# Kernel optimization log

Measured on AMD Instinct MI355X. Metric: run time of the kernel, lower is better.

Reference implementation:

```python
import jax, jax.numpy as jnp
import numpy as np

B, S, EMB, H = 2, 2048, 1024, 16
D = EMB // H  # per-head dim = 64
SCALE = 1.0 / np.sqrt(D).astype(np.float32)


def setup_inputs() -> dict:
    key = jax.random.key(0)
    ks = jax.random.split(key, 11)
    lim = 1.0 / np.sqrt(EMB).astype(np.float32)  # torch Linear default init range
    def lin(kw, kb):
        W = jax.random.uniform(kw, (EMB, EMB), jnp.float32, -lim, lim)
        b = jax.random.uniform(kb, (EMB,), jnp.float32, -lim, lim)
        return W, b
    Wq, bq = lin(ks[0], ks[1])
    Wk, bk = lin(ks[2], ks[3])
    Wv, bv = lin(ks[4], ks[5])
    Wo, bo = lin(ks[6], ks[7])
    xq = jax.random.normal(ks[8], (B, S, EMB), jnp.float32)
    xk = jax.random.normal(ks[9], (B, S, EMB), jnp.float32)
    xv = jax.random.normal(ks[10], (B, S, EMB), jnp.float32)
    mask = jnp.tril(jnp.ones((S, S), dtype=jnp.int32))  # causal mask; 0 -> blocked
    return {"xq": xq, "xk": xk, "xv": xv, "mask": mask,
            "Wq": Wq, "bq": bq, "Wk": Wk, "bk": bk,
            "Wv": Wv, "bv": bv, "Wo": Wo, "bo": bo}


def reference(xq, xk, xv, mask, Wq, bq, Wk, bk, Wv, bv, Wo, bo):
    # Projections (torch Linear: x @ W.T + b), then split heads: [B,S,E] -> [B,H,S,D]
    def split_heads(x):
        return x.reshape(B, S, H, D).transpose(0, 2, 1, 3)
    Q = split_heads(xq @ Wq.T + bq)
    K = split_heads(xk @ Wk.T + bk)
    V = split_heads(xv @ Wv.T + bv)
    scores = jnp.einsum("bhqd,bhkd->bhqk", Q, K) * SCALE  # [B,H,S,S]
    scores = jnp.where(mask[None, None, :, :] == 0, jnp.float32(-1e9), scores)
    attn = jax.nn.softmax(scores, axis=-1)  # softmax over key axis (dim=2 per-head in torch)
    res = jnp.einsum("bhqk,bhkd->bhqd", attn, V)
    res = res.transpose(0, 2, 1, 3).reshape(B, S, EMB)  # merge heads back (same slicing layout)
    return res @ Wo.T + bo
```

## Files before the change

### kernel.cpp

```cpp
#include <hip/hip_runtime.h>
#include <hip/hip_bf16.h>

#define BB   2
#define SS   2048
#define EMBD 1024
#define NH   16
#define HD   64
#define QSCALE 0.18033688011112042f
#define NEG_BIG (-1e30f)

typedef __bf16 bf16;
typedef float  floatx4 __attribute__((ext_vector_type(4)));
typedef __bf16 bf16x4  __attribute__((ext_vector_type(4)));
typedef __bf16 bf16x8  __attribute__((ext_vector_type(8)));

typedef const __attribute__((address_space(1))) void* gas_ptr;
typedef __attribute__((address_space(3))) void*       las_ptr;

__device__ __forceinline__ void gl_lds16(const void* g, void* l) {
    __builtin_amdgcn_global_load_lds((gas_ptr)g, (las_ptr)l, 16, 0, 0);
}

__device__ __forceinline__ bf16x8 cvt8(const float* p) {
    bf16x8 o;
#pragma unroll
    for (int j = 0; j < 8; j++) o[j] = (bf16)p[j];
    return o;
}

__global__ __launch_bounds__(256) void cvt_all(
    const float* __restrict__ xq, const float* __restrict__ xk,
    const float* __restrict__ xv, const float* __restrict__ Wq,
    const float* __restrict__ Wk, const float* __restrict__ Wv,
    const float* __restrict__ Wo, bf16* __restrict__ xqo,
    bf16* __restrict__ xko, bf16* __restrict__ xvo, bf16* __restrict__ Wqo,
    bf16* __restrict__ Wko, bf16* __restrict__ Wvo, bf16* __restrict__ Woo) {
    const int y = blockIdx.y;
    const float* src;
    bf16* dst;
    size_t n;
    const size_t NX = (size_t)BB * SS * EMBD;
    const size_t NW = (size_t)EMBD * EMBD;
    switch (y) {
        case 0: src = xq; dst = xqo; n = NX; break;
        case 1: src = xk; dst = xko; n = NX; break;
        case 2: src = xv; dst = xvo; n = NX; break;
        case 3: src = Wq; dst = Wqo; n = NW; break;
        case 4: src = Wk; dst = Wko; n = NW; break;
        case 5: src = Wv; dst = Wvo; n = NW; break;
        default: src = Wo; dst = Woo; n = NW; break;
    }
    const size_t stride = (size_t)gridDim.x * blockDim.x * 4;
    for (size_t i = ((size_t)blockIdx.x * blockDim.x + threadIdx.x) * 4;
         i < n; i += stride) {
        floatx4 v = *(const floatx4*)(src + i);
        bf16x4 o = {(bf16)v[0], (bf16)v[1], (bf16)v[2], (bf16)v[3]};
        *(bf16x4*)(dst + i) = o;
    }
}

extern __shared__ __align__(16) char smem[];

template <int MODE, int FM>
__device__ __forceinline__ void gemm_body(const bf16* __restrict__ A,
                                          const bf16* __restrict__ W,
                                          const float* __restrict__ bias,
                                          void* __restrict__ Ov,
                                          int mBase, int nBase, float oscale) {
    constexpr int BM = 32 * FM;
    constexpr int ABYTES = BM * 64 * 2;
    bf16* As = (bf16*)smem;
    bf16* Bs = (bf16*)(smem + ABYTES);

    const int t = threadIdx.x;
    const int l = t & 63, w = t >> 6;
    const int lm = l & 15, lq = l >> 4;
    const int K = 1024;
    const int wm = (w >> 1) * (16 * FM), wn = (w & 1) * 64;

    const floatx4 zero = {0.f, 0.f, 0.f, 0.f};
    floatx4 acc[FM][4];
#pragma unroll
    for (int i = 0; i < FM; i++)
#pragma unroll
        for (int j = 0; j < 4; j++) acc[i][j] = zero;

    for (int kb = 0; kb < K; kb += 64) {
        __syncthreads();
#pragma unroll
        for (int ia = 0; ia < FM; ia++) {
            int half = ia / (FM / 2 > 0 ? FM / 2 : 1);
            int rem  = (ia % (FM / 2 > 0 ? FM / 2 : 1)) * 256 + t;
            int row  = rem >> 2;
            int col  = half * 32 + (rem & 3) * 8;
            gl_lds16(A + (size_t)(mBase + row) * K + kb + col,
                     (char*)As + (ia * 256 + w * 64) * 16);
        }
#pragma unroll
        for (int i = 0; i < 4; i++) {
            int half = i >> 1;
            int rem  = (i & 1) * 256 + t;
            int row  = rem >> 2;
            int col  = half * 32 + (rem & 3) * 8;
            gl_lds16(W + (size_t)(nBase + row) * K + kb + col,
                     (char*)Bs + (i * 256 + w * 64) * 16);
        }
        __syncthreads();

#pragma unroll
        for (int half = 0; half < 2; half++) {
            const bf16* Ah = As + half * BM * 32;
            const bf16* Bh = Bs + half * 128 * 32;
            bf16x8 af[FM], bfv[4];
#pragma unroll
            for (int f = 0; f < FM; f++)
                af[f] = *(const bf16x8*)&Ah[(wm + f * 16 + lm) * 32 + lq * 8];
#pragma unroll
            for (int f = 0; f < 4; f++)
                bfv[f] = *(const bf16x8*)&Bh[(wn + f * 16 + lm) * 32 + lq * 8];
            if (MODE == 2) {
#pragma unroll
                for (int i = 0; i < 4; i++)
#pragma unroll
                    for (int j = 0; j < FM; j++)
                        acc[j][i] = __builtin_amdgcn_mfma_f32_16x16x32_bf16(
                            bfv[i], af[j], acc[j][i], 0, 0, 0);
            } else {
#pragma unroll
                for (int fm = 0; fm < FM; fm++)
#pragma unroll
                    for (int fn = 0; fn < 4; fn++)
                        acc[fm][fn] =
                            __builtin_amdgcn_mfma_f32_16x16x32_bf16(
                                af[fm], bfv[fn], acc[fm][fn], 0, 0, 0);
            }
        }
    }

    __syncthreads();
    float* rp = (float*)smem + w * (16 * 68);

    if (MODE != 2) {
        float bvv[4];
#pragma unroll
        for (int fn = 0; fn < 4; fn++)
            bvv[fn] = bias[nBase + wn + fn * 16 + lm];
#pragma unroll
        for (int fm = 0; fm < FM; fm++) {
#pragma unroll
            for (int fn = 0; fn < 4; fn++)
#pragma unroll
                for (int r = 0; r < 4; r++)
                    rp[(lq * 4 + r) * 68 + fn * 16 + lm] =
                        (acc[fm][fn][r] + bvv[fn]) * oscale;
            if (MODE == 0) {
                int row2 = l >> 3, col8 = l & 7;
                int h = (nBase + wn) >> 6;
#pragma unroll
                for (int p = 0; p < 2; p++) {
                    int row = p * 8 + row2;
                    int m = mBase + wm + fm * 16 + row;
                    int b = m >> 11, s = m & 2047;
                    bf16x8 o = cvt8(&rp[row * 68 + col8 * 8]);
                    *(bf16x8*)((bf16*)Ov +
                               (((size_t)(b * NH + h)) * SS + s) * HD +
                               col8 * 8) = o;
                }
            } else {
                int c4 = l & 15;
#pragma unroll
                for (int p = 0; p < 4; p++) {
                    int row = p * 4 + (l >> 4);
                    int m = mBase + wm + fm * 16 + row;
                    floatx4 o = *(const floatx4*)&rp[row * 68 + c4 * 4];
                    *(floatx4*)((float*)Ov + (size_t)m * EMBD + nBase + wn +
                                c4 * 4) = o;
                }
            }
        }
    } else {
        const int b = (mBase + wm) >> 11;
        const int sbase = (mBase + wm) & 2047;
#pragma unroll
        for (int i = 0; i < 4; i++) {
            float bv[4];
#pragma unroll
            for (int r = 0; r < 4; r++)
                bv[r] = bias[nBase + wn + i * 16 + lq * 4 + r];
#pragma unroll
            for (int j = 0; j < FM; j++)
#pragma unroll
                for (int r = 0; r < 4; r++)
                    rp[(lq * 4 + r) * 68 + j * 16 + lm] =
                        acc[j][i][r] + bv[r];
            int row2 = l >> 3, col8 = l & 7;
#pragma unroll
            for (int p = 0; p < 2; p++) {
                int row = p * 8 + row2;
                int n = nBase + wn + i * 16 + row;
                int h = n >> 6, d = n & 63;
                bf16x8 o = cvt8(&rp[row * 68 + col8 * 8]);
                *(bf16x8*)((bf16*)Ov +
                           ((size_t)(b * NH + h) * HD + d) * SS + sbase +
                           col8 * 8) = o;
            }
        }
    }
}

__global__ __launch_bounds__(256, 4) void gemm_qkv(
    const bf16* __restrict__ xq, const bf16* __restrict__ xk,
    const bf16* __restrict__ xv, const bf16* __restrict__ Wq,
    const bf16* __restrict__ Wk, const bf16* __restrict__ Wv,
    const float* __restrict__ bq, const float* __restrict__ bk,
    const float* __restrict__ bv, bf16* __restrict__ Qo,
    bf16* __restrict__ Ko, bf16* __restrict__ Vo) {
    const int z = blockIdx.z;
    const int mB = blockIdx.x * 128, nB = blockIdx.y * 128;
    if (z == 0)
        gemm_body<0, 4>(xq, Wq, bq, Qo, mB, nB, QSCALE);
    else if (z == 1)
        gemm_body<0, 4>(xk, Wk, bk, Ko, mB, nB, 1.0f);
    else
        gemm_body<2, 4>(xv, Wv, bv, Vo, mB, nB, 1.0f);
}

__global__ __launch_bounds__(256, 4) void gemm_out(
    const bf16* __restrict__ A, const bf16* __restrict__ W,
    const float* __restrict__ bias, float* __restrict__ O) {
    gemm_body<1, 2>(A, W, bias, O, blockIdx.x * 64, blockIdx.y * 128, 1.0f);
}

__global__ __launch_bounds__(256, 4) void attn_fwd(
    const bf16* __restrict__ Qg, const bf16* __restrict__ Kg,
    const bf16* __restrict__ Vtg, bf16* __restrict__ Oatt) {
    __shared__ __align__(16) bf16 Ks[64 * 72];
    __shared__ __align__(16) bf16 VT[64 * 72];
    __shared__ __align__(16) bf16 Ps[4][16 * 72];

    const int t = threadIdx.x;
    const int l = t & 63, w = t >> 6;
    const int lm = l & 15, lq = l >> 4;
    const int x = blockIdx.x;
    const int qt = 31 - (x >> 5);
    const int bh = (((x >> 3) & 3) << 3) | (x & 7);
    const size_t kbase = (size_t)bh * SS * HD;
    const size_t vbase = (size_t)bh * HD * SS;
    const int b = bh >> 4, h = bh & 15;
    const floatx4 zero = {0.f, 0.f, 0.f, 0.f};

    bf16x8 qa0, qa1;
    {
        const bf16* qp =
            Qg + kbase + (size_t)(qt * 64 + w * 16 + lm) * HD + lq * 8;
        qa0 = *(const bf16x8*)qp;
        qa1 = *(const bf16x8*)(qp + 32);
    }

    float m_i = NEG_BIG, l_i = 0.f;
    floatx4 od[4];
#pragma unroll
    for (int dt = 0; dt < 4; dt++) od[dt] = zero;

    const int qglob = qt * 64 + w * 16 + lm;

    bf16x8 kreg[2], vreg[2];
#pragma unroll
    for (int i = 0; i < 2; i++) {
        int idx = i * 256 + t;
        int row = idx >> 3;
        int col = (idx & 7) * 8;
        kreg[i] = *(const bf16x8*)(Kg + kbase + (size_t)row * HD + col);
        vreg[i] = *(const bf16x8*)(Vtg + vbase + (size_t)row * SS + col);
    }

    for (int kt = 0; kt <= qt; ++kt) {
        __syncthreads();
#pragma unroll
        for (int i = 0; i < 2; i++) {
            int idx = i * 256 + t;
            int row = idx >> 3;
            int col = (idx & 7) * 8;
            *(bf16x8*)&Ks[row * 72 + col] = kreg[i];
            *(bf16x8*)&VT[row * 72 + col] = vreg[i];
        }
        __syncthreads();
        if (kt < qt) {
#pragma unroll
            for (int i = 0; i < 2; i++) {
                int idx = i * 256 + t;
                int row = idx >> 3;
                int col = (idx & 7) * 8;
                kreg[i] = *(const bf16x8*)(
                    Kg + kbase + (size_t)((kt + 1) * 64 + row) * HD + col);
                vreg[i] = *(const bf16x8*)(
                    Vtg + vbase + (size_t)row * SS + (kt + 1) * 64 + col);
            }
        }

        floatx4 sc[4];
#pragma unroll
        for (int j0 = 0; j0 < 4; j0++) {
            int rowK = j0 * 16 + lm;
            bf16x8 k0 = *(const bf16x8*)&Ks[rowK * 72 + lq * 8];
            bf16x8 k1 = *(const bf16x8*)&Ks[rowK * 72 + 32 + lq * 8];
            floatx4 z = zero;
            z = __builtin_amdgcn_mfma_f32_16x16x32_bf16(k0, qa0, z, 0, 0, 0);
            z = __builtin_amdgcn_mfma_f32_16x16x32_bf16(k1, qa1, z, 0, 0, 0);
            sc[j0] = z;
        }
        if (kt == qt) {
#pragma unroll
            for (int j0 = 0; j0 < 4; j0++)
#pragma unroll
                for (int r = 0; r < 4; r++) {
                    int key = kt * 64 + j0 * 16 + lq * 4 + r;
                    if (key > qglob) sc[j0][r] = NEG_BIG;
                }
        }
        float mt = sc[0][0];
#pragma unroll
        for (int j0 = 0; j0 < 4; j0++)
#pragma unroll
            for (int r = 0; r < 4; r++) mt = fmaxf(mt, sc[j0][r]);
        mt = fmaxf(mt, __shfl_xor(mt, 16));
        mt = fmaxf(mt, __shfl_xor(mt, 32));
        float mnew = fmaxf(m_i, mt);
        float alpha = exp2f(m_i - mnew);
        m_i = mnew;
        float ps = 0.f;
#pragma unroll
        for (int j0 = 0; j0 < 4; j0++)
#pragma unroll
            for (int r = 0; r < 4; r++) {
                float p = exp2f(sc[j0][r] - mnew);
                sc[j0][r] = p;
                ps += p;
            }
        ps += __shfl_xor(ps, 16);
        ps += __shfl_xor(ps, 32);
        l_i = l_i * alpha + ps;
#pragma unroll
        for (int j0 = 0; j0 < 4; j0++) {
            bf16x4 pk = {(bf16)sc[j0][0], (bf16)sc[j0][1], (bf16)sc[j0][2],
                         (bf16)sc[j0][3]};
            *(bf16x4*)&Ps[w][lm * 72 + j0 * 16 + lq * 4] = pk;
        }
        float a0 = __shfl(alpha, lq * 4 + 0);
        float a1 = __shfl(alpha, lq * 4 + 1);
        float a2 = __shfl(alpha, lq * 4 + 2);
        float a3 = __shfl(alpha, lq * 4 + 3);
#pragma unroll
        for (int dt = 0; dt < 4; dt++) {
            od[dt][0] *= a0;
            od[dt][1] *= a1;
            od[dt][2] *= a2;
            od[dt][3] *= a3;
        }
        bf16x8 pa0 = *(const bf16x8*)&Ps[w][lm * 72 + lq * 8];
        bf16x8 pa1 = *(const bf16x8*)&Ps[w][lm * 72 + 32 + lq * 8];
#pragma unroll
        for (int dt = 0; dt < 4; dt++) {
            int rowD = dt * 16 + lm;
            bf16x8 v0 = *(const bf16x8*)&VT[rowD * 72 + lq * 8];
            bf16x8 v1 = *(const bf16x8*)&VT[rowD * 72 + 32 + lq * 8];
            od[dt] = __builtin_amdgcn_mfma_f32_16x16x32_bf16(pa0, v0, od[dt],
                                                             0, 0, 0);
            od[dt] = __builtin_amdgcn_mfma_f32_16x16x32_bf16(pa1, v1, od[dt],
                                                             0, 0, 0);
        }
    }

    float lr0 = __shfl(l_i, lq * 4 + 0);
    float lr1 = __shfl(l_i, lq * 4 + 1);
    float lr2 = __shfl(l_i, lq * 4 + 2);
    float lr3 = __shfl(l_i, lq * 4 + 3);
    float lr[4] = {lr0, lr1, lr2, lr3};
#pragma unroll
    for (int dt = 0; dt < 4; dt++) {
#pragma unroll
        for (int r = 0; r < 4; r++) {
            int s = qt * 64 + w * 16 + lq * 4 + r;
            float v = od[dt][r] / lr[r];
            Oatt[((size_t)(b * SS + s)) * EMBD + h * HD + dt * 16 + lm] =
                (bf16)v;
        }
    }
}

extern "C" void kernel_launch(void* const* d_in, const int* in_sizes, int n_in,
                              void* d_out, int out_size, void* d_ws,
                              size_t ws_size, hipStream_t stream) {
    const float* xq = (const float*)d_in[0];
    const float* xk = (const float*)d_in[1];
    const float* xv = (const float*)d_in[2];
    const float* Wq = (const float*)d_in[4];
    const float* bq = (const float*)d_in[5];
    const float* Wk = (const float*)d_in[6];
    const float* bk = (const float*)d_in[7];
    const float* Wv = (const float*)d_in[8];
    const float* bv = (const float*)d_in[9];
    const float* Wo = (const float*)d_in[10];
    const float* bo = (const float*)d_in[11];
    float* out = (float*)d_out;

    const size_t NX = (size_t)BB * SS * EMBD;
    const size_t NW = (size_t)EMBD * EMBD;
    bf16* Qw  = (bf16*)d_ws;
    bf16* Kw  = Qw + NX;
    bf16* Vw  = Kw + NX;
    bf16* Aw  = Vw + NX;
    bf16* xqb = Aw + NX;
    bf16* xkb = xqb + NX;
    bf16* xvb = xkb + NX;
    bf16* Wqb = xvb + NX;
    bf16* Wkb = Wqb + NW;
    bf16* Wvb = Wkb + NW;
    bf16* Wob = Wvb + NW;

    cvt_all<<<dim3(1024, 7), 256, 0, stream>>>(xq, xk, xv, Wq, Wk, Wv, Wo,
                                               xqb, xkb, xvb, Wqb, Wkb, Wvb,
                                               Wob);
    gemm_qkv<<<dim3(32, 8, 3), 256, 32768, stream>>>(
        xqb, xkb, xvb, Wqb, Wkb, Wvb, bq, bk, bv, Qw, Kw, Vw);
    attn_fwd<<<dim3(1024), 256, 0, stream>>>(Qw, Kw, Vw, Aw);
    gemm_out<<<dim3(64, 8), 256, 24576, stream>>>(Aw, Wob, bo, out);
}
```

Measured before the change: 229.7 us.

## Process 128-key chunks per iteration in attention and use fast exp2

The attention loop now consumes 128 keys per iteration instead of 64. This halves the number of barriers, LDS staging rounds and online-softmax rescale steps per query tile. It also switches to the hardware exp2 builtin and multiplies by a precomputed reciprocal of the row sum instead of dividing. In exchange, shared memory and register use grow (launch bounds lowered to 3 blocks per SM), and for even query tiles the last chunk computes and then masks 64 keys of wasted causal work.

```diff
diff --git a/kernel.cpp b/kernel.cpp
--- a/kernel.cpp
+++ b/kernel.cpp
@@ -231,12 +231,12 @@
     gemm_body<1, 2>(A, W, bias, O, blockIdx.x * 64, blockIdx.y * 128, 1.0f);
 }
 
-__global__ __launch_bounds__(256, 4) void attn_fwd(
+__global__ __launch_bounds__(256, 3) void attn_fwd(
     const bf16* __restrict__ Qg, const bf16* __restrict__ Kg,
     const bf16* __restrict__ Vtg, bf16* __restrict__ Oatt) {
-    __shared__ __align__(16) bf16 Ks[64 * 72];
-    __shared__ __align__(16) bf16 VT[64 * 72];
-    __shared__ __align__(16) bf16 Ps[4][16 * 72];
+    __shared__ __align__(16) bf16 Ks[128 * 72];
+    __shared__ __align__(16) bf16 VT[64 * 136];
+    __shared__ __align__(16) bf16 Ps[4][16 * 136];
 
     const int t = threadIdx.x;
     const int l = t & 63, w = t >> 6;
@@ -244,6 +244,7 @@
     const int x = blockIdx.x;
     const int qt = 31 - (x >> 5);
     const int bh = (((x >> 3) & 3) << 3) | (x & 7);
+    const int nch = (qt >> 1) + 1;
     const size_t kbase = (size_t)bh * SS * HD;
     const size_t vbase = (size_t)bh * HD * SS;
     const int b = bh >> 4, h = bh & 15;
@@ -264,43 +265,43 @@
 
     const int qglob = qt * 64 + w * 16 + lm;
 
-    bf16x8 kreg[2], vreg[2];
-#pragma unroll
-    for (int i = 0; i < 2; i++) {
+    bf16x8 kreg[4], vreg[4];
+#pragma unroll
+    for (int i = 0; i < 4; i++) {
         int idx = i * 256 + t;
-        int row = idx >> 3;
-        int col = (idx & 7) * 8;
-        kreg[i] = *(const bf16x8*)(Kg + kbase + (size_t)row * HD + col);
-        vreg[i] = *(const bf16x8*)(Vtg + vbase + (size_t)row * SS + col);
-    }
-
-    for (int kt = 0; kt <= qt; ++kt) {
+        int rowK = idx >> 3, colK = (idx & 7) * 8;
+        kreg[i] = *(const bf16x8*)(Kg + kbase + (size_t)rowK * HD + colK);
+        int dV = idx >> 4, keyb = (idx & 15) * 8;
+        vreg[i] = *(const bf16x8*)(Vtg + vbase + (size_t)dV * SS + keyb);
+    }
+
+    for (int kt = 0; kt < nch; ++kt) {
         __syncthreads();
 #pragma unroll
-        for (int i = 0; i < 2; i++) {
+        for (int i = 0; i < 4; i++) {
             int idx = i * 256 + t;
-            int row = idx >> 3;
-            int col = (idx & 7) * 8;
-            *(bf16x8*)&Ks[row * 72 + col] = kreg[i];
-            *(bf16x8*)&VT[row * 72 + col] = vreg[i];
+            int rowK = idx >> 3, colK = (idx & 7) * 8;
+            *(bf16x8*)&Ks[rowK * 72 + colK] = kreg[i];
+            int dV = idx >> 4, keyb = (idx & 15) * 8;
+            *(bf16x8*)&VT[dV * 136 + keyb] = vreg[i];
         }
         __syncthreads();
-        if (kt < qt) {
-#pragma unroll
-            for (int i = 0; i < 2; i++) {
+        if (kt < nch - 1) {
+#pragma unroll
+            for (int i = 0; i < 4; i++) {
                 int idx = i * 256 + t;
-                int row = idx >> 3;
-                int col = (idx & 7) * 8;
+                int rowK = idx >> 3, colK = (idx & 7) * 8;
                 kreg[i] = *(const bf16x8*)(
-                    Kg + kbase + (size_t)((kt + 1) * 64 + row) * HD + col);
+                    Kg + kbase + (size_t)((kt + 1) * 128 + rowK) * HD + colK);
+                int dV = idx >> 4, keyb = (idx & 15) * 8;
                 vreg[i] = *(const bf16x8*)(
-                    Vtg + vbase + (size_t)row * SS + (kt + 1) * 64 + col);
-            }
-        }
-
-        floatx4 sc[4];
-#pragma unroll
-        for (int j0 = 0; j0 < 4; j0++) {
+                    Vtg + vbase + (size_t)dV * SS + (kt + 1) * 128 + keyb);
+            }
+        }
+
+        floatx4 sc[8];
+#pragma unroll
+        for (int j0 = 0; j0 < 8; j0++) {
             int rowK = j0 * 16 + lm;
             bf16x8 k0 = *(const bf16x8*)&Ks[rowK * 72 + lq * 8];
             bf16x8 k1 = *(const bf16x8*)&Ks[rowK * 72 + 32 + lq * 8];
@@ -309,31 +310,31 @@
             z = __builtin_amdgcn_mfma_f32_16x16x32_bf16(k1, qa1, z, 0, 0, 0);
             sc[j0] = z;
         }
-        if (kt == qt) {
-#pragma unroll
-            for (int j0 = 0; j0 < 4; j0++)
+        if (kt == nch - 1) {
+#pragma unroll
+            for (int j0 = 0; j0 < 8; j0++)
 #pragma unroll
                 for (int r = 0; r < 4; r++) {
-                    int key = kt * 64 + j0 * 16 + lq * 4 + r;
+                    int key = kt * 128 + j0 * 16 + lq * 4 + r;
                     if (key > qglob) sc[j0][r] = NEG_BIG;
                 }
         }
         float mt = sc[0][0];
 #pragma unroll
-        for (int j0 = 0; j0 < 4; j0++)
+        for (int j0 = 0; j0 < 8; j0++)
 #pragma unroll
             for (int r = 0; r < 4; r++) mt = fmaxf(mt, sc[j0][r]);
         mt = fmaxf(mt, __shfl_xor(mt, 16));
         mt = fmaxf(mt, __shfl_xor(mt, 32));
         float mnew = fmaxf(m_i, mt);
-        float alpha = exp2f(m_i - mnew);
+        float alpha = __builtin_amdgcn_exp2f(m_i - mnew);
         m_i = mnew;
         float ps = 0.f;
 #pragma unroll
-        for (int j0 = 0; j0 < 4; j0++)
+        for (int j0 = 0; j0 < 8; j0++)
 #pragma unroll
             for (int r = 0; r < 4; r++) {
-                float p = exp2f(sc[j0][r] - mnew);
+                float p = __builtin_amdgcn_exp2f(sc[j0][r] - mnew);
                 sc[j0][r] = p;
                 ps += p;
             }
@@ -341,10 +342,10 @@
         ps += __shfl_xor(ps, 32);
         l_i = l_i * alpha + ps;
 #pragma unroll
-        for (int j0 = 0; j0 < 4; j0++) {
+        for (int j0 = 0; j0 < 8; j0++) {
             bf16x4 pk = {(bf16)sc[j0][0], (bf16)sc[j0][1], (bf16)sc[j0][2],
                          (bf16)sc[j0][3]};
-            *(bf16x4*)&Ps[w][lm * 72 + j0 * 16 + lq * 4] = pk;
+            *(bf16x4*)&Ps[w][lm * 136 + j0 * 16 + lq * 4] = pk;
         }
         float a0 = __shfl(alpha, lq * 4 + 0);
         float a1 = __shfl(alpha, lq * 4 + 1);
@@ -357,31 +358,35 @@
             od[dt][2] *= a2;
             od[dt][3] *= a3;
         }
-        bf16x8 pa0 = *(const bf16x8*)&Ps[w][lm * 72 + lq * 8];
-        bf16x8 pa1 = *(const bf16x8*)&Ps[w][lm * 72 + 32 + lq * 8];
+        bf16x8 pa[4];
+#pragma unroll
+        for (int s = 0; s < 4; s++)
+            pa[s] = *(const bf16x8*)&Ps[w][lm * 136 + s * 32 + lq * 8];
 #pragma unroll
         for (int dt = 0; dt < 4; dt++) {
             int rowD = dt * 16 + lm;
-            bf16x8 v0 = *(const bf16x8*)&VT[rowD * 72 + lq * 8];
-            bf16x8 v1 = *(const bf16x8*)&VT[rowD * 72 + 32 + lq * 8];
-            od[dt] = __builtin_amdgcn_mfma_f32_16x16x32_bf16(pa0, v0, od[dt],
-                                                             0, 0, 0);
-            od[dt] = __builtin_amdgcn_mfma_f32_16x16x32_bf16(pa1, v1, od[dt],
-                                                             0, 0, 0);
-        }
-    }
-
-    float lr0 = __shfl(l_i, lq * 4 + 0);
-    float lr1 = __shfl(l_i, lq * 4 + 1);
-    float lr2 = __shfl(l_i, lq * 4 + 2);
-    float lr3 = __shfl(l_i, lq * 4 + 3);
+#pragma unroll
+            for (int s = 0; s < 4; s++) {
+                bf16x8 v = *(const bf16x8*)&VT[rowD * 136 + s * 32 + lq * 8];
+                od[dt] = __builtin_amdgcn_mfma_f32_16x16x32_bf16(pa[s], v,
+                                                                 od[dt], 0, 0,
+                                                                 0);
+            }
+        }
+    }
+
+    float linv = 1.0f / l_i;
+    float lr0 = __shfl(linv, lq * 4 + 0);
+    float lr1 = __shfl(linv, lq * 4 + 1);
+    float lr2 = __shfl(linv, lq * 4 + 2);
+    float lr3 = __shfl(linv, lq * 4 + 3);
     float lr[4] = {lr0, lr1, lr2, lr3};
 #pragma unroll
     for (int dt = 0; dt < 4; dt++) {
 #pragma unroll
         for (int r = 0; r < 4; r++) {
             int s = qt * 64 + w * 16 + lq * 4 + r;
-            float v = od[dt][r] / lr[r];
+            float v = od[dt][r] * lr[r];
             Oatt[((size_t)(b * SS + s)) * EMBD + h * HD + dt * 16 + lm] =
                 (bf16)v;
         }
```

Result: faster. 225.0 us (-2.0%).
